# Optimization experiments

Measured on AMD Instinct MI355X. Metric: run time of the kernel, lower is better.

The kernel has to match this reference:

```python
import jax, jax.numpy as jnp
import numpy as np

B, S, H, A, F = 16, 512, 768, 12, 3072
DH = H // A  # 64
EPS = 1e-5

def layernorm(x, w, b):
    mu = jnp.mean(x, axis=-1, keepdims=True)
    var = jnp.mean(jnp.square(x - mu), axis=-1, keepdims=True)
    return (x - mu) * jax.lax.rsqrt(var + EPS) * w + b

def setup_inputs() -> dict:
    key = jax.random.key(0)
    ks = jax.random.split(key, 12)
    std = 0.02
    inp = {
        "X": jax.random.normal(ks[0], (B, S, H), jnp.float32),
        "mask": jax.random.randint(ks[1], (B, S), 0, 2, jnp.int32),
        "WQ": jax.random.normal(ks[2], (H, H), jnp.float32) * std,
        "bQ": jnp.zeros((H,), jnp.float32),
        "WK": jax.random.normal(ks[3], (H, H), jnp.float32) * std,
        "bK": jnp.zeros((H,), jnp.float32),
        "WV": jax.random.normal(ks[4], (H, H), jnp.float32) * std,
        "bV": jnp.zeros((H,), jnp.float32),
        "WO": jax.random.normal(ks[5], (H, H), jnp.float32) * std,
        "bO": jnp.zeros((H,), jnp.float32),
        "ln1_w": jnp.ones((H,), jnp.float32),
        "ln1_b": jnp.zeros((H,), jnp.float32),
        "W1": jax.random.normal(ks[6], (H, F), jnp.float32) * std,
        "b1": jnp.zeros((F,), jnp.float32),
        "W2": jax.random.normal(ks[7], (F, H), jnp.float32) * std,
        "b2": jnp.zeros((H,), jnp.float32),
        "ln2_w": jnp.ones((H,), jnp.float32),
        "ln2_b": jnp.zeros((H,), jnp.float32),
    }
    return inp

def reference(X, mask, WQ, bQ, WK, bK, WV, bV, WO, bO, ln1_w, ln1_b, W1, b1, W2, b2, ln2_w, ln2_b):
    # --- multi-head self-attention (pretrained-weights branch, faithful reshapes) ---
    Q = (X @ WQ + bQ).reshape(B, A, S, DH)
    K = (X @ WK + bK).reshape(B, A, S, DH)
    V = (X @ WV + bV).reshape(B, A, S, DH)
    scores = jnp.einsum('bhqd,bhkd->bhqk', Q, K) / jnp.sqrt(jnp.float32(DH))
    scores = jnp.where(mask[:, None, None, :] == 0, -jnp.inf, scores)
    attn = jax.nn.softmax(scores, axis=-1)
    Z = jnp.einsum('bhqk,bhkd->bhqd', attn, V).reshape(B, S, H)
    attn_out = Z @ WO + bO
    # residual + LN (dropout is identity in eval)
    X = layernorm(attn_out + X, ln1_w, ln1_b)
    # --- FFN with exact GELU ---
    ffn = jax.nn.gelu(X @ W1 + b1, approximate=False) @ W2 + b2
    X = layernorm(ffn + X, ln2_w, ln2_b)
    return X
```

## Files before the change

kernel.cpp:

```cpp
#include <hip/hip_runtime.h>
#include <hip/hip_bf16.h>


using bf16_t = __hip_bfloat16;
typedef __bf16 bf16x8 __attribute__((ext_vector_type(8)));
typedef float f32x4 __attribute__((ext_vector_type(4)));

__device__ __forceinline__ float b2f(bf16_t v) { return __bfloat162float(v); }
__device__ __forceinline__ bf16_t f2b(float v) { return __float2bfloat16(v); }
__device__ __forceinline__ ushort f2bu(float v) { bf16_t b = f2b(v); return *(ushort*)&b; }

__device__ __forceinline__ void glds16(const ushort* g, ushort* l) {
    __builtin_amdgcn_global_load_lds(
        (const __attribute__((address_space(1))) unsigned int*)g,
        (__attribute__((address_space(3))) unsigned int*)l, 16, 0, 0);
}

__global__ __launch_bounds__(256) void cast_f32_bf16(
    const float* __restrict__ in, bf16_t* __restrict__ out)
{
    size_t i = ((size_t)blockIdx.x * 256 + threadIdx.x) * 8;
    float4 a = *(const float4*)(in + i);
    float4 b = *(const float4*)(in + i + 4);
#pragma unroll
    for (int j = 0; j < 4; ++j) {
        out[i + j]     = f2b(((const float*)&a)[j]);
        out[i + 4 + j] = f2b(((const float*)&b)[j]);
    }
}

__global__ __launch_bounds__(256) void transpose_cast(
    const float* __restrict__ in, bf16_t* __restrict__ out, int R, int C)
{
    __shared__ float t[64][65];
    int r0 = blockIdx.y * 64, c0 = blockIdx.x * 64;
    int tr = threadIdx.x >> 6, tc = threadIdx.x & 63;
#pragma unroll 4
    for (int i = 0; i < 16; ++i) {
        int r = i * 4 + tr;
        t[r][tc] = in[(size_t)(r0 + r) * C + c0 + tc];
    }
    __syncthreads();
#pragma unroll 4
    for (int i = 0; i < 16; ++i) {
        int r = i * 4 + tr;
        out[(size_t)(c0 + r) * R + r0 + tc] = f2b(t[tc][r]);
    }
}

__global__ __launch_bounds__(256) void transpose_bf(
    const ushort* __restrict__ in, ushort* __restrict__ out,
    int R, int C, long inB, long outB)
{
    __shared__ ushort t[64][65];
    const ushort* ip = in + (size_t)blockIdx.z * inB;
    ushort* op = out + (size_t)blockIdx.z * outB;
    int r0 = blockIdx.y * 64, c0 = blockIdx.x * 64;
    int tr = threadIdx.x >> 6, tc = threadIdx.x & 63;
#pragma unroll 4
    for (int i = 0; i < 16; ++i) {
        int r = i * 4 + tr;
        t[r][tc] = ip[(size_t)(r0 + r) * C + c0 + tc];
    }
    __syncthreads();
#pragma unroll 4
    for (int i = 0; i < 16; ++i) {
        int r = i * 4 + tr;
        op[(size_t)(c0 + r) * R + r0 + tc] = t[tc][r];
    }
}

template <int EPI>
__global__ __launch_bounds__(256) void gemm128(
    const bf16_t* __restrict__ A, const bf16_t* __restrict__ Bt,
    const float* __restrict__ bias, const void* __restrict__ res,
    void* __restrict__ Cv, int K, int lda, int ldb, int ldc)
{
    __shared__ ushort lA[128 * 32];
    __shared__ ushort lB[128 * 32];
    const int tid = threadIdx.x;
    const int l = tid & 63, w = tid >> 6;
    const int l16 = l & 15, quad = l >> 4;
    const int m0 = blockIdx.x * 128, n0 = blockIdx.y * 128;

    const int srow = tid >> 2;
    const int scol = (((tid & 3) ^ ((tid >> 3) & 3)) << 3);
    const ushort* gA = (const ushort*)A + (size_t)(m0 + srow) * lda + scol;
    const ushort* gB = (const ushort*)Bt + (size_t)(n0 + srow) * ldb + scol;
    const size_t skipA = (size_t)64 * lda, skipB = (size_t)64 * ldb;
    ushort* dA = lA + tid * 8;
    ushort* dB = lB + tid * 8;

    f32x4 acc[4][4] = {};
    const int arow = (w & 1) * 64;
    const int brow = (w >> 1) * 64;
    const int pch = ((quad ^ ((l16 >> 1) & 3)) << 3);

    for (int k0 = 0; k0 < K; k0 += 32) {
        __syncthreads();
        glds16(gA + k0,         dA);
        glds16(gA + k0 + skipA, dA + 2048);
        glds16(gB + k0,         dB);
        glds16(gB + k0 + skipB, dB + 2048);
        __syncthreads();
        bf16x8 bfr[4];
#pragma unroll
        for (int ni = 0; ni < 4; ++ni)
            bfr[ni] = *(const bf16x8*)&lB[(brow + ni * 16 + l16) * 32 + pch];
#pragma unroll
        for (int mi = 0; mi < 4; ++mi) {
            bf16x8 afr = *(const bf16x8*)&lA[(arow + mi * 16 + l16) * 32 + pch];
#pragma unroll
            for (int ni = 0; ni < 4; ++ni)
                acc[mi][ni] = __builtin_amdgcn_mfma_f32_16x16x32_bf16(afr, bfr[ni], acc[mi][ni], 0, 0, 0);
        }
    }

    float bv[4];
#pragma unroll
    for (int ni = 0; ni < 4; ++ni) bv[ni] = bias ? bias[n0 + brow + ni * 16 + l16] : 0.f;

#pragma unroll
    for (int mi = 0; mi < 4; ++mi) {
#pragma unroll
        for (int ni = 0; ni < 4; ++ni) {
            int n = n0 + brow + ni * 16 + l16;
#pragma unroll
            for (int r = 0; r < 4; ++r) {
                int m = m0 + arow + mi * 16 + quad * 4 + r;
                float v = acc[mi][ni][r] + bv[ni];
                if constexpr (EPI == 1) {
                    v = 0.5f * v * (1.f + erff(v * 0.70710678118654752f));
                } else if constexpr (EPI == 2) {
                    v += ((const float*)res)[(size_t)m * ldc + n];
                } else if constexpr (EPI == 5) {
                    v += b2f(((const bf16_t*)res)[(size_t)m * ldc + n]);
                }
                if constexpr (EPI == 5) {
                    ((float*)Cv)[(size_t)m * ldc + n] = v;
                } else {
                    ((bf16_t*)Cv)[(size_t)m * ldc + n] = f2b(v);
                }
            }
        }
    }
}

__global__ __launch_bounds__(256) void flash_kernel(
    const bf16_t* __restrict__ Q, const bf16_t* __restrict__ Kx,
    const bf16_t* __restrict__ Vt, const int* __restrict__ mask,
    bf16_t* __restrict__ Z)
{
    __shared__ ushort lK[64 * 64];
    __shared__ ushort lV[64 * 64];
    __shared__ ushort lP[64 * 72];

    const int h = blockIdx.y;
    const int q0 = blockIdx.x * 64;
    const ushort* Qh = (const ushort*)Q + (size_t)h * 32768;
    const ushort* Kh = (const ushort*)Kx + (size_t)h * 32768;
    const ushort* Vh = (const ushort*)Vt + (size_t)h * 32768;
    const int* mk = mask + (h / 12) * 512;
    ushort* Zh = (ushort*)Z + (size_t)h * 32768;

    const int tid = threadIdx.x;
    const int l = tid & 63, w = tid >> 6;
    const int l16 = l & 15, quad = l >> 4;

    bf16x8 qfr[2];
#pragma unroll
    for (int kk = 0; kk < 2; ++kk)
        qfr[kk] = *(const bf16x8*)(Qh + (size_t)(q0 + w * 16 + l16) * 64 + kk * 32 + quad * 8);

    const int c8p = tid & 7;
    const int kr0 = tid >> 3;
    float m_i[4] = {-1e30f, -1e30f, -1e30f, -1e30f};
    float l_i[4] = {0.f, 0.f, 0.f, 0.f};
    f32x4 o4[4] = {};

    const int sw = (quad << 2);

    for (int kt = 0; kt < 8; ++kt) {
#pragma unroll
        for (int p = 0; p < 2; ++p) {
            int row = kr0 + p * 32;
            int c8l = c8p ^ (row & 7);
            glds16(Kh + (size_t)(kt * 64 + row) * 64 + c8l * 8, lK + (p * 256 + tid) * 8);
            glds16(Vh + (size_t)row * 512 + kt * 64 + c8l * 8, lV + (p * 256 + tid) * 8);
        }
        __syncthreads();

        f32x4 s4[4] = {};
#pragma unroll
        for (int kk = 0; kk < 2; ++kk) {
#pragma unroll
            for (int nt = 0; nt < 4; ++nt) {
                int rr = nt * 16 + l16;
                bf16x8 bfr = *(const bf16x8*)&lK[rr * 64 + (((kk * 4 + quad) ^ (l16 & 7)) << 3)];
                s4[nt] = __builtin_amdgcn_mfma_f32_16x16x32_bf16(qfr[kk], bfr, s4[nt], 0, 0, 0);
            }
        }

        bool mz[4];
#pragma unroll
        for (int nt = 0; nt < 4; ++nt) mz[nt] = (mk[kt * 64 + nt * 16 + l16] == 0);
        float pv[4][4];
#pragma unroll
        for (int r = 0; r < 4; ++r) {
            float rm = -1e30f;
#pragma unroll
            for (int nt = 0; nt < 4; ++nt) {
                float v = mz[nt] ? -1e30f : s4[nt][r] * 0.125f;
                pv[nt][r] = v;
                rm = fmaxf(rm, v);
            }
#pragma unroll
            for (int off = 1; off < 16; off <<= 1) rm = fmaxf(rm, __shfl_xor(rm, off));
            float mn = fmaxf(m_i[r], rm);
            float al = __expf(m_i[r] - mn);
            float rs = 0.f;
#pragma unroll
            for (int nt = 0; nt < 4; ++nt) {
                float e = __expf(pv[nt][r] - mn);
                pv[nt][r] = e;
                rs += e;
            }
#pragma unroll
            for (int off = 1; off < 16; off <<= 1) rs += __shfl_xor(rs, off);
            l_i[r] = l_i[r] * al + rs;
            m_i[r] = mn;
#pragma unroll
            for (int dt = 0; dt < 4; ++dt) o4[dt][r] *= al;
        }

#pragma unroll
        for (int nt = 0; nt < 4; ++nt)
#pragma unroll
            for (int r = 0; r < 4; ++r)
                lP[(w * 16 + quad * 4 + r) * 72 + nt * 16 + l16] = f2bu(pv[nt][r]);
        __syncthreads();

#pragma unroll
        for (int kk = 0; kk < 2; ++kk) {
            bf16x8 pafr = *(const bf16x8*)&lP[(w * 16 + l16) * 72 + kk * 32 + quad * 8];
#pragma unroll
            for (int dt = 0; dt < 4; ++dt) {
                bf16x8 bvfr = *(const bf16x8*)&lV[(dt * 16 + l16) * 64 + (((kk * 4 + quad) ^ (l16 & 7)) << 3)];
                o4[dt] = __builtin_amdgcn_mfma_f32_16x16x32_bf16(pafr, bvfr, o4[dt], 0, 0, 0);
            }
        }
        __syncthreads();
    }

    float inv[4];
#pragma unroll
    for (int r = 0; r < 4; ++r) inv[r] = 1.f / l_i[r];
#pragma unroll
    for (int dt = 0; dt < 4; ++dt)
#pragma unroll
        for (int r = 0; r < 4; ++r)
            Zh[(size_t)(q0 + w * 16 + quad * 4 + r) * 64 + dt * 16 + l16] = f2bu(o4[dt][r] * inv[r]);
}

__device__ __forceinline__ float to_f(float v)  { return v; }
__device__ __forceinline__ float to_f(bf16_t v) { return b2f(v); }
__device__ __forceinline__ void from_f(float& d, float v)  { d = v; }
__device__ __forceinline__ void from_f(bf16_t& d, float v) { d = f2b(v); }

template <typename TI, typename TO>
__global__ __launch_bounds__(256) void layernorm_kernel(
    const TI* __restrict__ X, const float* __restrict__ w,
    const float* __restrict__ b, TO* __restrict__ out)
{
    const TI* x = X + (size_t)blockIdx.x * 768;
    TO* o = out + (size_t)blockIdx.x * 768;
    int t = threadIdx.x;
    float v[3];
    float s = 0.f, sq = 0.f;
#pragma unroll
    for (int i = 0; i < 3; ++i) {
        v[i] = to_f(x[t + i * 256]);
        s += v[i]; sq += v[i] * v[i];
    }
#pragma unroll
    for (int off = 32; off; off >>= 1) { s += __shfl_xor(s, off); sq += __shfl_xor(sq, off); }
    __shared__ float s1[4], s2[4];
    int wave = t >> 6, lane = t & 63;
    if (lane == 0) { s1[wave] = s; s2[wave] = sq; }
    __syncthreads();
    s  = s1[0] + s1[1] + s1[2] + s1[3];
    sq = s2[0] + s2[1] + s2[2] + s2[3];
    float mu  = s * (1.f / 768.f);
    float var = sq * (1.f / 768.f) - mu * mu;
    float rs  = rsqrtf(var + 1e-5f);
#pragma unroll
    for (int i = 0; i < 3; ++i)
        from_f(o[t + i * 256], (v[i] - mu) * rs * w[t + i * 256] + b[t + i * 256]);
}

extern "C" void kernel_launch(void* const* d_in, const int* in_sizes, int n_in,
                              void* d_out, int out_size, void* d_ws, size_t ws_size,
                              hipStream_t stream)
{
    const float* X    = (const float*)d_in[0];
    const int*   mask = (const int*)  d_in[1];
    const float* WQ   = (const float*)d_in[2];
    const float* bQ   = (const float*)d_in[3];
    const float* WK   = (const float*)d_in[4];
    const float* bK   = (const float*)d_in[5];
    const float* WV   = (const float*)d_in[6];
    const float* bV   = (const float*)d_in[7];
    const float* WO   = (const float*)d_in[8];
    const float* bO   = (const float*)d_in[9];
    const float* ln1w = (const float*)d_in[10];
    const float* ln1b = (const float*)d_in[11];
    const float* W1   = (const float*)d_in[12];
    const float* b1   = (const float*)d_in[13];
    const float* W2   = (const float*)d_in[14];
    const float* b2   = (const float*)d_in[15];
    const float* ln2w = (const float*)d_in[16];
    const float* ln2b = (const float*)d_in[17];
    float* out = (float*)d_out;

    bf16_t* ws = (bf16_t*)d_ws;
    bf16_t* WQt = ws;
    bf16_t* WKt = WQt + 589824;
    bf16_t* WVt = WKt + 589824;
    bf16_t* WOt = WVt + 589824;
    bf16_t* W1t = WOt + 589824;
    bf16_t* W2t = W1t + 2359296;
    bf16_t* Vb  = W2t + 2359296;
    bf16_t* Xb  = Vb  + 6291456;
    bf16_t* Qb  = Xb  + 6291456;
    bf16_t* Kb  = Qb  + 6291456;
    bf16_t* Vt  = Kb  + 6291456;
    bf16_t* Zb = Qb;
    bf16_t* Y1 = Xb;
    bf16_t* X1 = Vb;
    bf16_t* Hb = Xb;

    cast_f32_bf16<<<3072, 256, 0, stream>>>(X, Xb);
    transpose_cast<<<dim3(12, 12), 256, 0, stream>>>(WQ, WQt, 768, 768);
    transpose_cast<<<dim3(12, 12), 256, 0, stream>>>(WK, WKt, 768, 768);
    transpose_cast<<<dim3(12, 12), 256, 0, stream>>>(WV, WVt, 768, 768);
    transpose_cast<<<dim3(12, 12), 256, 0, stream>>>(WO, WOt, 768, 768);
    transpose_cast<<<dim3(48, 12), 256, 0, stream>>>(W1, W1t, 768, 3072);
    transpose_cast<<<dim3(12, 48), 256, 0, stream>>>(W2, W2t, 3072, 768);

    gemm128<0><<<dim3(64, 6), 256, 0, stream>>>(Xb, WQt, bQ, nullptr, Qb, 768, 768, 768, 768);
    gemm128<0><<<dim3(64, 6), 256, 0, stream>>>(Xb, WKt, bK, nullptr, Kb, 768, 768, 768, 768);
    gemm128<0><<<dim3(64, 6), 256, 0, stream>>>(Xb, WVt, bV, nullptr, Vb, 768, 768, 768, 768);

    transpose_bf<<<dim3(1, 8, 192), 256, 0, stream>>>((const ushort*)Vb, (ushort*)Vt, 512, 64, 32768, 32768);

    flash_kernel<<<dim3(8, 192), 256, 0, stream>>>(Qb, Kb, Vt, mask, Zb);

    gemm128<2><<<dim3(64, 6), 256, 0, stream>>>(Zb, WOt, bO, X, Y1, 768, 768, 768, 768);
    layernorm_kernel<bf16_t, bf16_t><<<8192, 256, 0, stream>>>(Y1, ln1w, ln1b, X1);

    gemm128<1><<<dim3(64, 24), 256, 0, stream>>>(X1, W1t, b1, nullptr, Hb, 768, 768, 768, 3072);
    gemm128<5><<<dim3(64, 6), 256, 0, stream>>>(Hb, W2t, b2, X1, out, 3072, 3072, 3072, 768);
    layernorm_kernel<float, float><<<8192, 256, 0, stream>>>(out, ln2w, ln2b, out);
}
```

Measured before the change: 444.8 us.

## Merge prep kernels, fuse QKV GEMM, use 64-wide N tiles for N=768 GEMMs

Replaces the seven weight-transpose and X-cast launches with a single prep kernel. Concatenates WQ/WK/WV so one GEMM launch produces Q, K and V, with an epilogue that scatters the outputs into separate buffers. Adds an NTILE template parameter so the out-proj and FFN2 GEMMs (N=768) run with 128x64 tiles, doubling their block count from 384 to 768 to fill the GPU better. The cost is less data reuse per tile on those GEMMs.

After: 394.2 us. 11.4% less time.

```diff
diff --git a/kernel.cpp b/kernel.cpp
--- a/kernel.cpp
+++ b/kernel.cpp
@@ -16,25 +16,13 @@
         (__attribute__((address_space(3))) unsigned int*)l, 16, 0, 0);
 }
 
-__global__ __launch_bounds__(256) void cast_f32_bf16(
-    const float* __restrict__ in, bf16_t* __restrict__ out)
-{
-    size_t i = ((size_t)blockIdx.x * 256 + threadIdx.x) * 8;
-    float4 a = *(const float4*)(in + i);
-    float4 b = *(const float4*)(in + i + 4);
-#pragma unroll
-    for (int j = 0; j < 4; ++j) {
-        out[i + j]     = f2b(((const float*)&a)[j]);
-        out[i + 4 + j] = f2b(((const float*)&b)[j]);
-    }
-}
-
-__global__ __launch_bounds__(256) void transpose_cast(
-    const float* __restrict__ in, bf16_t* __restrict__ out, int R, int C)
-{
-    __shared__ float t[64][65];
-    int r0 = blockIdx.y * 64, c0 = blockIdx.x * 64;
-    int tr = threadIdx.x >> 6, tc = threadIdx.x & 63;
+__device__ __forceinline__ void tr_tile(const float* __restrict__ in,
+                                        bf16_t* __restrict__ out,
+                                        int R, int C, int tx, int ty,
+                                        float (*t)[65], int tid)
+{
+    int r0 = ty * 64, c0 = tx * 64;
+    int tr = tid >> 6, tc = tid & 63;
 #pragma unroll 4
     for (int i = 0; i < 16; ++i) {
         int r = i * 4 + tr;
@@ -45,6 +33,45 @@
     for (int i = 0; i < 16; ++i) {
         int r = i * 4 + tr;
         out[(size_t)(c0 + r) * R + r0 + tc] = f2b(t[tc][r]);
+    }
+}
+
+__global__ __launch_bounds__(256) void prep_kernel(
+    const float* __restrict__ WQ, const float* __restrict__ WK,
+    const float* __restrict__ WV, const float* __restrict__ WO,
+    const float* __restrict__ W1, const float* __restrict__ W2,
+    const float* __restrict__ bQ, const float* __restrict__ bK,
+    const float* __restrict__ bV, const float* __restrict__ X,
+    bf16_t* __restrict__ Wqkv, bf16_t* __restrict__ WOt,
+    bf16_t* __restrict__ W1t, bf16_t* __restrict__ W2t,
+    float* __restrict__ bcat, bf16_t* __restrict__ Xb)
+{
+    __shared__ float t[64][65];
+    const int blk = blockIdx.x, tid = threadIdx.x;
+    if (blk < 576) {
+        int m = blk / 144, tt = blk % 144;
+        const float* in = (m == 0) ? WQ : (m == 1) ? WK : (m == 2) ? WV : WO;
+        bf16_t* out = (m == 0) ? Wqkv : (m == 1) ? Wqkv + 589824
+                    : (m == 2) ? Wqkv + 1179648 : WOt;
+        tr_tile(in, out, 768, 768, tt % 12, tt / 12, t, tid);
+    } else if (blk < 1152) {
+        int tt = blk - 576;
+        tr_tile(W1, W1t, 768, 3072, tt % 48, tt / 48, t, tid);
+    } else if (blk < 1728) {
+        int tt = blk - 1152;
+        tr_tile(W2, W2t, 3072, 768, tt % 12, tt / 12, t, tid);
+    } else if (blk == 1728) {
+        for (int i = tid; i < 2304; i += 256)
+            bcat[i] = (i < 768) ? bQ[i] : (i < 1536) ? bK[i - 768] : bV[i - 1536];
+    } else {
+        size_t i = ((size_t)(blk - 1729) * 256 + tid) * 8;
+        float4 a = *(const float4*)(X + i);
+        float4 b = *(const float4*)(X + i + 4);
+#pragma unroll
+        for (int j = 0; j < 4; ++j) {
+            Xb[i + j]     = f2b(((const float*)&a)[j]);
+            Xb[i + 4 + j] = f2b(((const float*)&b)[j]);
+        }
     }
 }
 
@@ -70,18 +97,19 @@
     }
 }
 
-template <int EPI>
+template <int EPI, int NTILE>
 __global__ __launch_bounds__(256) void gemm128(
     const bf16_t* __restrict__ A, const bf16_t* __restrict__ Bt,
     const float* __restrict__ bias, const void* __restrict__ res,
     void* __restrict__ Cv, int K, int lda, int ldb, int ldc)
 {
     __shared__ ushort lA[128 * 32];
-    __shared__ ushort lB[128 * 32];
+    __shared__ ushort lB[NTILE * 32];
+    constexpr int NI = NTILE / 32;
     const int tid = threadIdx.x;
     const int l = tid & 63, w = tid >> 6;
     const int l16 = l & 15, quad = l >> 4;
-    const int m0 = blockIdx.x * 128, n0 = blockIdx.y * 128;
+    const int m0 = blockIdx.x * 128, n0 = blockIdx.y * NTILE;
 
     const int srow = tid >> 2;
     const int scol = (((tid & 3) ^ ((tid >> 3) & 3)) << 3);
@@ -91,9 +119,9 @@
     ushort* dA = lA + tid * 8;
     ushort* dB = lB + tid * 8;
 
-    f32x4 acc[4][4] = {};
+    f32x4 acc[4][NI] = {};
     const int arow = (w & 1) * 64;
-    const int brow = (w >> 1) * 64;
+    const int brow = (w >> 1) * (NTILE / 2);
     const int pch = ((quad ^ ((l16 >> 1) & 3)) << 3);
 
     for (int k0 = 0; k0 < K; k0 += 32) {
@@ -101,29 +129,36 @@
         glds16(gA + k0,         dA);
         glds16(gA + k0 + skipA, dA + 2048);
         glds16(gB + k0,         dB);
-        glds16(gB + k0 + skipB, dB + 2048);
-        __syncthreads();
-        bf16x8 bfr[4];
-#pragma unroll
-        for (int ni = 0; ni < 4; ++ni)
+        if constexpr (NTILE == 128) glds16(gB + k0 + skipB, dB + 2048);
+        __syncthreads();
+        bf16x8 bfr[NI];
+#pragma unroll
+        for (int ni = 0; ni < NI; ++ni)
             bfr[ni] = *(const bf16x8*)&lB[(brow + ni * 16 + l16) * 32 + pch];
 #pragma unroll
         for (int mi = 0; mi < 4; ++mi) {
             bf16x8 afr = *(const bf16x8*)&lA[(arow + mi * 16 + l16) * 32 + pch];
 #pragma unroll
-            for (int ni = 0; ni < 4; ++ni)
+            for (int ni = 0; ni < NI; ++ni)
                 acc[mi][ni] = __builtin_amdgcn_mfma_f32_16x16x32_bf16(afr, bfr[ni], acc[mi][ni], 0, 0, 0);
         }
     }
 
-    float bv[4];
-#pragma unroll
-    for (int ni = 0; ni < 4; ++ni) bv[ni] = bias ? bias[n0 + brow + ni * 16 + l16] : 0.f;
+    float bv[NI];
+#pragma unroll
+    for (int ni = 0; ni < NI; ++ni) bv[ni] = bias[n0 + brow + ni * 16 + l16];
+
+    bf16_t* Cseg = nullptr;
+    int nloc0 = 0;
+    if constexpr (EPI == 6) {
+        Cseg = (bf16_t*)Cv + (size_t)(n0 / 768) * 6291456;
+        nloc0 = (n0 % 768) + brow;
+    }
 
 #pragma unroll
     for (int mi = 0; mi < 4; ++mi) {
 #pragma unroll
-        for (int ni = 0; ni < 4; ++ni) {
+        for (int ni = 0; ni < NI; ++ni) {
             int n = n0 + brow + ni * 16 + l16;
 #pragma unroll
             for (int r = 0; r < 4; ++r) {
@@ -138,6 +173,8 @@
                 }
                 if constexpr (EPI == 5) {
                     ((float*)Cv)[(size_t)m * ldc + n] = v;
+                } else if constexpr (EPI == 6) {
+                    Cseg[(size_t)m * 768 + nloc0 + ni * 16 + l16] = f2b(v);
                 } else {
                     ((bf16_t*)Cv)[(size_t)m * ldc + n] = f2b(v);
                 }
@@ -177,8 +214,6 @@
     float m_i[4] = {-1e30f, -1e30f, -1e30f, -1e30f};
     float l_i[4] = {0.f, 0.f, 0.f, 0.f};
     f32x4 o4[4] = {};
-
-    const int sw = (quad << 2);
 
     for (int kt = 0; kt < 8; ++kt) {
 #pragma unroll
@@ -322,43 +357,40 @@
     const float* ln2b = (const float*)d_in[17];
     float* out = (float*)d_out;
 
-    bf16_t* ws = (bf16_t*)d_ws;
-    bf16_t* WQt = ws;
-    bf16_t* WKt = WQt + 589824;
-    bf16_t* WVt = WKt + 589824;
-    bf16_t* WOt = WVt + 589824;
-    bf16_t* W1t = WOt + 589824;
-    bf16_t* W2t = W1t + 2359296;
-    bf16_t* Vb  = W2t + 2359296;
-    bf16_t* Xb  = Vb  + 6291456;
-    bf16_t* Qb  = Xb  + 6291456;
-    bf16_t* Kb  = Qb  + 6291456;
-    bf16_t* Vt  = Kb  + 6291456;
+    bf16_t* ws   = (bf16_t*)d_ws;
+    bf16_t* Wqkv = ws;
+    bf16_t* WOt  = Wqkv + 1769472;
+    bf16_t* W1t  = WOt + 589824;
+    bf16_t* W2t  = W1t + 2359296;
+    float*  bcat = (float*)(W2t + 2359296);
+    bf16_t* Qb   = W2t + 2359296 + 4608;
+    bf16_t* Kb   = Qb + 6291456;
+    bf16_t* Vb   = Kb + 6291456;
+    bf16_t* Xb   = Vb + 6291456;
+    bf16_t* Vt   = Xb + 6291456;
     bf16_t* Zb = Qb;
     bf16_t* Y1 = Xb;
-    bf16_t* X1 = Vb;
-    bf16_t* Hb = Xb;
-
-    cast_f32_bf16<<<3072, 256, 0, stream>>>(X, Xb);
-    transpose_cast<<<dim3(12, 12), 256, 0, stream>>>(WQ, WQt, 768, 768);
-    transpose_cast<<<dim3(12, 12), 256, 0, stream>>>(WK, WKt, 768, 768);
-    transpose_cast<<<dim3(12, 12), 256, 0, stream>>>(WV, WVt, 768, 768);
-    transpose_cast<<<dim3(12, 12), 256, 0, stream>>>(WO, WOt, 768, 768);
-    transpose_cast<<<dim3(48, 12), 256, 0, stream>>>(W1, W1t, 768, 3072);
-    transpose_cast<<<dim3(12, 48), 256, 0, stream>>>(W2, W2t, 3072, 768);
-
-    gemm128<0><<<dim3(64, 6), 256, 0, stream>>>(Xb, WQt, bQ, nullptr, Qb, 768, 768, 768, 768);
-    gemm128<0><<<dim3(64, 6), 256, 0, stream>>>(Xb, WKt, bK, nullptr, Kb, 768, 768, 768, 768);
-    gemm128<0><<<dim3(64, 6), 256, 0, stream>>>(Xb, WVt, bV, nullptr, Vb, 768, 768, 768, 768);
-
-    transpose_bf<<<dim3(1, 8, 192), 256, 0, stream>>>((const ushort*)Vb, (ushort*)Vt, 512, 64, 32768, 32768);
+    bf16_t* X1 = Qb;
+    bf16_t* Hb = Kb;
+
+    prep_kernel<<<4801, 256, 0, stream>>>(WQ, WK, WV, WO, W1, W2, bQ, bK, bV, X,
+                                          Wqkv, WOt, W1t, W2t, bcat, Xb);
+
+    gemm128<6, 128><<<dim3(64, 18), 256, 0, stream>>>(Xb, Wqkv, bcat, nullptr, Qb,
+                                                      768, 768, 768, 768);
+
+    transpose_bf<<<dim3(1, 8, 192), 256, 0, stream>>>((const ushort*)Vb, (ushort*)Vt,
+                                                      512, 64, 32768, 32768);
 
     flash_kernel<<<dim3(8, 192), 256, 0, stream>>>(Qb, Kb, Vt, mask, Zb);
 
-    gemm128<2><<<dim3(64, 6), 256, 0, stream>>>(Zb, WOt, bO, X, Y1, 768, 768, 768, 768);
+    gemm128<2, 64><<<dim3(64, 12), 256, 0, stream>>>(Zb, WOt, bO, X, Y1,
+                                                     768, 768, 768, 768);
     layernorm_kernel<bf16_t, bf16_t><<<8192, 256, 0, stream>>>(Y1, ln1w, ln1b, X1);
 
-    gemm128<1><<<dim3(64, 24), 256, 0, stream>>>(X1, W1t, b1, nullptr, Hb, 768, 768, 768, 3072);
-    gemm128<5><<<dim3(64, 6), 256, 0, stream>>>(Hb, W2t, b2, X1, out, 3072, 3072, 3072, 768);
+    gemm128<1, 128><<<dim3(64, 24), 256, 0, stream>>>(X1, W1t, b1, nullptr, Hb,
+                                                      768, 768, 768, 3072);
+    gemm128<5, 64><<<dim3(64, 12), 256, 0, stream>>>(Hb, W2t, b2, X1, out,
+                                                     3072, 3072, 3072, 768);
     layernorm_kernel<float, float><<<8192, 256, 0, stream>>>(out, ln2w, ln2b, out);
 }
```
